# Kernel tuning notes

Hardware: AMD Instinct MI355X
Metric: run time of the kernel (lower is better)

The kernel has to match this reference:

```python
import jax, jax.numpy as jnp
import numpy as np

DIM = 512
HEADS = 8
DIM_HEAD = 64
INNER = HEADS * DIM_HEAD  # 512
B, N = 4, 2048


def setup_inputs() -> dict:
    key = jax.random.key(0)
    k1, k2, k3, k4 = jax.random.split(key, 4)
    x = jax.random.normal(k1, (B, N, DIM), dtype=jnp.float32)
    # nn.Linear(dim, inner*3, bias=False): weight [3*inner, dim]; store transposed [dim, 3*inner]
    w_qkv = jax.random.normal(k2, (DIM, 3 * INNER), dtype=jnp.float32) / np.sqrt(DIM)
    w_out = jax.random.normal(k3, (INNER, DIM), dtype=jnp.float32) / np.sqrt(INNER)
    b_out = jax.random.normal(k4, (DIM,), dtype=jnp.float32) * 0.01
    return {"x": x, "w_qkv": w_qkv, "w_out": w_out, "b_out": b_out}


def reference(x, w_qkv, w_out, b_out):
    b, n, _ = x.shape
    scale = DIM_HEAD ** -0.5
    qkv = x @ w_qkv  # [b, n, 3*inner]
    q, k, v = jnp.split(qkv, 3, axis=-1)
    # [b, n, h, d] -> [b, h, n, d]
    reshape = lambda t: t.reshape(b, n, HEADS, DIM_HEAD).transpose(0, 2, 1, 3)
    q, k, v = reshape(q), reshape(k), reshape(v)
    dots = jnp.einsum('bhid,bhjd->bhij', q, k) * scale  # [b, h, n, n]
    attn = jax.nn.softmax(dots, axis=-1)
    out = jnp.einsum('bhij,bhjd->bhid', attn, v)  # [b, h, n, d]
    out = out.transpose(0, 2, 1, 3).reshape(b, n, INNER)
    return out @ w_out + b_out  # dropout is identity at inference
```

## Files before the change

### kernel.cpp

```cpp
#include <hip/hip_runtime.h>
#include <hip/hip_bf16.h>
#include <cstdint>

#define DEV __device__ __forceinline__

typedef __attribute__((ext_vector_type(8))) __bf16 bf16x8;
typedef __attribute__((ext_vector_type(4))) float floatx4;
typedef __attribute__((ext_vector_type(4))) short shortx4;
typedef __attribute__((ext_vector_type(8))) short shortx8;

constexpr float QSCALE = 0.18033688011112042f;

DEV unsigned short f2b(float f) {
  union { float f; unsigned u; } v; v.f = f;
  return (unsigned short)((v.u + 0x7fffu + ((v.u >> 16) & 1u)) >> 16);
}

#if defined(__has_builtin) && __has_builtin(__builtin_amdgcn_cvt_pk_bf16_f32)
DEV unsigned pk2(float a, float b) {
  typedef __attribute__((ext_vector_type(2))) __bf16 bf2;
  union { bf2 v; unsigned u; } u;
  u.v = __builtin_amdgcn_cvt_pk_bf16_f32(a, b);
  return u.u;
}
#else
DEV unsigned pk2(float a, float b) {
  return (unsigned)f2b(a) | ((unsigned)f2b(b) << 16);
}
#endif

#if defined(__has_builtin) && __has_builtin(__builtin_amdgcn_exp2f)
DEV float fexp2(float x) { return __builtin_amdgcn_exp2f(x); }
#else
DEV float fexp2(float x) { return exp2f(x); }
#endif

DEV floatx4 mfma16(bf16x8 a, bf16x8 b, floatx4 c) {
  return __builtin_amdgcn_mfma_f32_16x16x32_bf16(a, b, c, 0, 0, 0);
}

#define GLD_LDS16(gp, lp)                                                          \
  __builtin_amdgcn_global_load_lds(                                                \
      (const __attribute__((address_space(1))) void*)(gp),                         \
      (__attribute__((address_space(3))) void*)(lp), 16, 0, 0)

__global__ void cvt_f32_bf16(const float* __restrict__ in,
                             unsigned short* __restrict__ out, int n4) {
  int i = blockIdx.x * 256 + threadIdx.x;
  if (i >= n4) return;
  floatx4 f = ((const floatx4*)in)[i];
  shortx4 s;
  s[0] = (short)f2b(f[0]); s[1] = (short)f2b(f[1]);
  s[2] = (short)f2b(f[2]); s[3] = (short)f2b(f[3]);
  ((shortx4*)out)[i] = s;
}

__global__ void tcvt(const float* __restrict__ in, unsigned short* __restrict__ out,
                     int R, int C) {
  __shared__ float tile[32][33];
  int tx = threadIdx.x & 31, ty = threadIdx.x >> 5;
  int r0 = blockIdx.y * 32, c0 = blockIdx.x * 32;
#pragma unroll
  for (int i = 0; i < 4; i++) {
    int rr = ty + i * 8;
    tile[rr][tx] = in[(size_t)(r0 + rr) * C + c0 + tx];
  }
  __syncthreads();
#pragma unroll
  for (int i = 0; i < 4; i++) {
    int rr = ty + i * 8;
    out[(size_t)(c0 + rr) * R + r0 + tx] = f2b(tile[tx][rr]);
  }
}

__global__ void vtrans(const unsigned short* __restrict__ in,
                       unsigned short* __restrict__ out) {
  __shared__ unsigned short Ts[64][68];
  const int t = threadIdx.x;
  const int n0 = blockIdx.x * 64;
  const size_t base = (size_t)blockIdx.y * (2048 * 64);
  const int rr = t >> 4, c4 = (t & 15) * 4;
#pragma unroll
  for (int j = 0; j < 4; j++) {
    int row = j * 16 + rr;
    *(shortx4*)(&Ts[row][c4]) =
        *(const shortx4*)(in + base + (size_t)(n0 + row) * 64 + c4);
  }
  __syncthreads();
#pragma unroll
  for (int j = 0; j < 4; j++) {
    int d = j * 16 + rr;
    shortx4 s;
#pragma unroll
    for (int i = 0; i < 4; i++) s[i] = (short)Ts[c4 + i][d];
    *(shortx4*)(out + base + (size_t)d * 2048 + n0 + c4) = s;
  }
}

template <int MODE>
__global__ __launch_bounds__(256, 2) void gemm_bt(
    const unsigned short* __restrict__ A, const unsigned short* __restrict__ Bt, int K,
    unsigned short* __restrict__ qg, unsigned short* __restrict__ kg,
    unsigned short* __restrict__ vg, float* __restrict__ outF,
    const float* __restrict__ bias) {
  __shared__ __align__(16) unsigned short Xs[128 * 32];
  __shared__ __align__(16) unsigned short Ws[128 * 32];
  const int tid = threadIdx.x;
  const int lane = tid & 63, wid = tid >> 6;
  const int g = lane >> 4, r = lane & 15;
  const int m0 = blockIdx.y * 128, n0 = blockIdx.x * 128;
  const int wm = (wid & 1) * 64, wn = (wid >> 1) * 64;

  floatx4 acc[4][4] = {};

  const int c0i = tid, c1i = 256 + tid;
  const int row0 = c0i >> 2, kb0 = (c0i & 3) ^ ((row0 >> 1) & 3);
  const int row1 = c1i >> 2, kb1 = (c1i & 3) ^ ((row1 >> 1) & 3);
  const unsigned ldsOff0 = (unsigned)(wid * 64) * 16;
  const unsigned ldsOff1 = (unsigned)(256 + wid * 64) * 16;

  for (int kt = 0; kt < K; kt += 32) {
    GLD_LDS16(A + (size_t)(m0 + row0) * K + kt + kb0 * 8, (char*)Xs + ldsOff0);
    GLD_LDS16(A + (size_t)(m0 + row1) * K + kt + kb1 * 8, (char*)Xs + ldsOff1);
    GLD_LDS16(Bt + (size_t)(n0 + row0) * K + kt + kb0 * 8, (char*)Ws + ldsOff0);
    GLD_LDS16(Bt + (size_t)(n0 + row1) * K + kt + kb1 * 8, (char*)Ws + ldsOff1);
    __syncthreads();
    bf16x8 a[4], b[4];
#pragma unroll
    for (int t = 0; t < 4; t++) {
      int rowA = wm + t * 16 + r;
      a[t] = *(const bf16x8*)(Xs + rowA * 32 + (g ^ ((rowA >> 1) & 3)) * 8);
      int rowB = wn + t * 16 + r;
      b[t] = *(const bf16x8*)(Ws + rowB * 32 + (g ^ ((rowB >> 1) & 3)) * 8);
    }
#pragma unroll
    for (int mt = 0; mt < 4; mt++)
#pragma unroll
      for (int nt = 0; nt < 4; nt++)
        acc[mt][nt] = mfma16(a[mt], b[nt], acc[mt][nt]);
    __syncthreads();
  }

#pragma unroll
  for (int mt = 0; mt < 4; mt++)
#pragma unroll
    for (int nt = 0; nt < 4; nt++) {
      int col = n0 + wn + nt * 16 + r;
#pragma unroll
      for (int e = 0; e < 4; e++) {
        int rowm = m0 + wm + mt * 16 + g * 4 + e;
        float v = acc[mt][nt][e];
        if (MODE == 0) {
          int which = col >> 9;
          int h = (col >> 6) & 7, d = col & 63;
          int bb = rowm >> 11, n = rowm & 2047;
          size_t idx = ((size_t)(bb * 8 + h) * 2048 + n) * 64 + d;
          if (which == 0) qg[idx] = f2b(v * QSCALE);
          else if (which == 1) kg[idx] = f2b(v);
          else vg[idx] = f2b(v);
        } else {
          outF[(size_t)rowm * 512 + col] = v + bias[col];
        }
      }
    }
}

__global__ __launch_bounds__(256, 2) void attn(
    const unsigned short* __restrict__ qg, const unsigned short* __restrict__ kg,
    const unsigned short* __restrict__ vtg, unsigned short* __restrict__ ao) {
  __shared__ __align__(16) unsigned short Ks[2 * 64 * 64];
  __shared__ __align__(16) unsigned short Vt[2 * 64 * 64];
  __shared__ __align__(16) unsigned short Pn[4 * 64 * 64];
  const int tid = threadIdx.x, lane = tid & 63, wid = tid >> 6;
  const int g = lane >> 4, r = lane & 15, r7 = r & 7;
  const int wq = wid & 1, wk = wid >> 1;
  const int bh = blockIdx.y, q0 = blockIdx.x * 128;
  const size_t base = (size_t)bh * (2048 * 64);
  const int chunk = (lane & 7) ^ ((lane >> 3) & 7);
  const int srow = lane >> 3;

  bf16x8 bq[4][2];
#pragma unroll
  for (int nt = 0; nt < 4; nt++)
#pragma unroll
    for (int kc = 0; kc < 2; kc++)
      bq[nt][kc] = *(const bf16x8*)(qg + base +
                                    (size_t)(q0 + wq * 64 + nt * 16 + r) * 64 +
                                    kc * 32 + g * 8);

  bf16x8 vones;
#pragma unroll
  for (int i = 0; i < 8; i++) vones[i] = (__bf16)1.0f;

  floatx4 o[4][4] = {};
  floatx4 lacc[4] = {};

  for (int it = 0; it < 16; it++) {
    const int n0 = it * 128 + wk * 64;
    if (it) __syncthreads();
    if (wq == 0) {
#pragma unroll
      for (int j = 0; j < 8; j++) {
        int row = j * 8 + srow;
        GLD_LDS16(kg + base + (size_t)(n0 + row) * 64 + chunk * 8,
                  (char*)Ks + wk * 8192 + j * 1024);
      }
    } else {
#pragma unroll
      for (int j = 0; j < 8; j++) {
        int row = j * 8 + srow;
        GLD_LDS16(vtg + base + (size_t)row * 2048 + n0 + chunk * 8,
                  (char*)Vt + wk * 8192 + j * 1024);
      }
    }
    __syncthreads();

    floatx4 st[4][4] = {};
#pragma unroll
    for (int kc = 0; kc < 2; kc++)
#pragma unroll
      for (int mt = 0; mt < 4; mt++) {
        bf16x8 ak = *(const bf16x8*)(Ks + wk * 4096 + (mt * 16 + r) * 64 +
                                     ((kc * 4 + g) ^ r7) * 8);
#pragma unroll
        for (int nt = 0; nt < 4; nt++)
          st[mt][nt] = mfma16(ak, bq[nt][kc], st[mt][nt]);
      }

#pragma unroll
    for (int mt = 0; mt < 4; mt++)
#pragma unroll
      for (int nt = 0; nt < 4; nt++) {
        unsigned lo = pk2(fexp2(st[mt][nt][0]), fexp2(st[mt][nt][1]));
        unsigned hi = pk2(fexp2(st[mt][nt][2]), fexp2(st[mt][nt][3]));
        unsigned long long w = (unsigned long long)lo |
                               ((unsigned long long)hi << 32);
        int prow = nt * 16 + r;
        int slot = (mt * 2 + (g >> 1)) ^ r7;
        *(unsigned long long*)((char*)Pn + wid * 8192 + prow * 128 + slot * 16 +
                               (g & 1) * 8) = w;
      }

#pragma unroll
    for (int kc = 0; kc < 2; kc++) {
      bf16x8 bv[4];
#pragma unroll
      for (int nt = 0; nt < 4; nt++)
        bv[nt] = *(const bf16x8*)(Vt + wk * 4096 + (nt * 16 + r) * 64 +
                                  ((kc * 4 + g) ^ r7) * 8);
#pragma unroll
      for (int mt = 0; mt < 4; mt++) {
        bf16x8 ap = *(const bf16x8*)(Pn + wid * 4096 + (mt * 16 + r) * 64 +
                                     ((kc * 4 + g) ^ r7) * 8);
        lacc[mt] = mfma16(ap, vones, lacc[mt]);
#pragma unroll
        for (int nt = 0; nt < 4; nt++)
          o[mt][nt] = mfma16(ap, bv[nt], o[mt][nt]);
      }
    }
  }

  __syncthreads();
  float* fP = (float*)Pn;
  float* fL = (float*)Ks;
  if (wk == 1) {
#pragma unroll
    for (int mt = 0; mt < 4; mt++) {
      *(floatx4*)&fL[wq * 1024 + mt * 256 + lane * 4] = lacc[mt];
#pragma unroll
      for (int nt = 0; nt < 4; nt++)
        *(floatx4*)&fP[wq * 4096 + (mt * 4 + nt) * 256 + lane * 4] = o[mt][nt];
    }
  }
  __syncthreads();
  if (wk == 0) {
    const int bb = bh >> 3, h = bh & 7;
#pragma unroll
    for (int mt = 0; mt < 4; mt++) {
      floatx4 lt = lacc[mt] + *(floatx4*)&fL[wq * 1024 + mt * 256 + lane * 4];
      floatx4 il;
#pragma unroll
      for (int e = 0; e < 4; e++) il[e] = 1.f / lt[e];
#pragma unroll
      for (int nt = 0; nt < 4; nt++) {
        floatx4 oo = o[mt][nt] +
                     *(floatx4*)&fP[wq * 4096 + (mt * 4 + nt) * 256 + lane * 4];
        int d = nt * 16 + r;
#pragma unroll
        for (int e = 0; e < 4; e++) {
          int qrow = q0 + wq * 64 + mt * 16 + g * 4 + e;
          ao[((size_t)(bb * 2048 + qrow)) * 512 + h * 64 + d] =
              f2b(oo[e] * il[e]);
        }
      }
    }
  }
}

extern "C" void kernel_launch(void* const* d_in, const int* in_sizes, int n_in,
                              void* d_out, int out_size, void* d_ws, size_t ws_size,
                              hipStream_t stream) {
  const float* x = (const float*)d_in[0];
  const float* w_qkv = (const float*)d_in[1];
  const float* w_out = (const float*)d_in[2];
  const float* b_out = (const float*)d_in[3];
  float* out = (float*)d_out;

  unsigned short* wsp = (unsigned short*)d_ws;
  unsigned short* xb = wsp;
  unsigned short* wqkvt = xb + (size_t)8192 * 512;
  unsigned short* woutt = wqkvt + (size_t)1536 * 512;
  unsigned short* qg = woutt + (size_t)512 * 512;
  unsigned short* kg = qg + (size_t)32 * 2048 * 64;
  unsigned short* vg = kg + (size_t)32 * 2048 * 64;
  unsigned short* vtg = vg + (size_t)32 * 2048 * 64;
  unsigned short* ao = vg;

  cvt_f32_bf16<<<4096, 256, 0, stream>>>(x, xb, 8192 * 512 / 4);
  tcvt<<<dim3(48, 16), 256, 0, stream>>>(w_qkv, wqkvt, 512, 1536);
  tcvt<<<dim3(16, 16), 256, 0, stream>>>(w_out, woutt, 512, 512);
  gemm_bt<0><<<dim3(12, 64), 256, 0, stream>>>(xb, wqkvt, 512, qg, kg, vg,
                                               nullptr, nullptr);
  vtrans<<<dim3(32, 32), 256, 0, stream>>>(vg, vtg);
  attn<<<dim3(16, 32), 256, 0, stream>>>(qg, kg, vtg, ao);
  gemm_bt<1><<<dim3(4, 64), 256, 0, stream>>>(ao, woutt, 512, nullptr, nullptr,
                                              nullptr, out, b_out);
}
```

Baseline: 171.8 us.

## Fuse V transpose into QKV GEMM, register-resident attention, coalesced epilogues

```diff
diff --git a/kernel.cpp b/kernel.cpp
--- a/kernel.cpp
+++ b/kernel.cpp
@@ -73,38 +73,15 @@
   }
 }
 
-__global__ void vtrans(const unsigned short* __restrict__ in,
-                       unsigned short* __restrict__ out) {
-  __shared__ unsigned short Ts[64][68];
-  const int t = threadIdx.x;
-  const int n0 = blockIdx.x * 64;
-  const size_t base = (size_t)blockIdx.y * (2048 * 64);
-  const int rr = t >> 4, c4 = (t & 15) * 4;
-#pragma unroll
-  for (int j = 0; j < 4; j++) {
-    int row = j * 16 + rr;
-    *(shortx4*)(&Ts[row][c4]) =
-        *(const shortx4*)(in + base + (size_t)(n0 + row) * 64 + c4);
-  }
-  __syncthreads();
-#pragma unroll
-  for (int j = 0; j < 4; j++) {
-    int d = j * 16 + rr;
-    shortx4 s;
-#pragma unroll
-    for (int i = 0; i < 4; i++) s[i] = (short)Ts[c4 + i][d];
-    *(shortx4*)(out + base + (size_t)d * 2048 + n0 + c4) = s;
-  }
-}
-
 template <int MODE>
 __global__ __launch_bounds__(256, 2) void gemm_bt(
     const unsigned short* __restrict__ A, const unsigned short* __restrict__ Bt, int K,
     unsigned short* __restrict__ qg, unsigned short* __restrict__ kg,
-    unsigned short* __restrict__ vg, float* __restrict__ outF,
+    unsigned short* __restrict__ vtg, float* __restrict__ outF,
     const float* __restrict__ bias) {
-  __shared__ __align__(16) unsigned short Xs[128 * 32];
-  __shared__ __align__(16) unsigned short Ws[128 * 32];
+  __shared__ __align__(16) unsigned short smem[128 * 136];
+  unsigned short* Xs = smem;
+  unsigned short* Ws = smem + 4096;
   const int tid = threadIdx.x;
   const int lane = tid & 63, wid = tid >> 6;
   const int g = lane >> 4, r = lane & 15;
@@ -141,51 +118,99 @@
     __syncthreads();
   }
 
-#pragma unroll
-  for (int mt = 0; mt < 4; mt++)
-#pragma unroll
-    for (int nt = 0; nt < 4; nt++) {
-      int col = n0 + wn + nt * 16 + r;
-#pragma unroll
-      for (int e = 0; e < 4; e++) {
-        int rowm = m0 + wm + mt * 16 + g * 4 + e;
-        float v = acc[mt][nt][e];
-        if (MODE == 0) {
-          int which = col >> 9;
-          int h = (col >> 6) & 7, d = col & 63;
-          int bb = rowm >> 11, n = rowm & 2047;
-          size_t idx = ((size_t)(bb * 8 + h) * 2048 + n) * 64 + d;
-          if (which == 0) qg[idx] = f2b(v * QSCALE);
-          else if (which == 1) kg[idx] = f2b(v);
-          else vg[idx] = f2b(v);
-        } else {
-          outF[(size_t)rowm * 512 + col] = v + bias[col];
+  if (MODE == 0) {
+    const int which = blockIdx.x >> 2;
+    if (which == 2) {
+      const int tokbase = m0 + wm;
+      const int bb = tokbase >> 11, nb = tokbase & 2047;
+#pragma unroll
+      for (int mt = 0; mt < 4; mt++) {
+        const int s = (mt >> 1) * 32 + g * 8 + (mt & 1) * 4;
+#pragma unroll
+        for (int nt = 0; nt < 4; nt++) {
+          int vcol = n0 + wn + nt * 16 + r - 1024;
+          int h = vcol >> 6, d = vcol & 63;
+          unsigned long long w =
+              (unsigned long long)pk2(acc[mt][nt][0], acc[mt][nt][1]) |
+              ((unsigned long long)pk2(acc[mt][nt][2], acc[mt][nt][3]) << 32);
+          *(unsigned long long*)(vtg + ((size_t)(bb * 8 + h) * 64 + d) * 2048 +
+                                 nb + s) = w;
         }
       }
-    }
-}
-
-__global__ __launch_bounds__(256, 2) void attn(
+    } else {
+      const float sc = (which == 0) ? QSCALE : 1.f;
+      unsigned short* dst = (which == 0) ? qg : kg;
+#pragma unroll
+      for (int mt = 0; mt < 4; mt++)
+#pragma unroll
+        for (int nt = 0; nt < 4; nt++) {
+          int col = wn + nt * 16 + r;
+#pragma unroll
+          for (int e = 0; e < 4; e++) {
+            int row = wm + mt * 16 + g * 4 + e;
+            smem[row * 136 + col] = f2b(acc[mt][nt][e] * sc);
+          }
+        }
+      __syncthreads();
+#pragma unroll
+      for (int it = 0; it < 8; it++) {
+        int c = it * 256 + tid;
+        int row = c >> 4, cc = c & 15;
+        shortx8 v = *(const shortx8*)(smem + row * 136 + cc * 8);
+        int gq = n0 + cc * 8;
+        int h = (gq >> 6) & 7, d0 = gq & 63;
+        int tok = m0 + row, bb = tok >> 11, n = tok & 2047;
+        *(shortx8*)(dst + ((size_t)(bb * 8 + h) * 2048 + n) * 64 + d0) = v;
+      }
+    }
+  } else {
+    float* ftile = (float*)smem;
+#pragma unroll
+    for (int half = 0; half < 2; half++) {
+      if (half) __syncthreads();
+#pragma unroll
+      for (int mi = 0; mi < 2; mi++) {
+        int mt = half * 2 + mi;
+#pragma unroll
+        for (int nt = 0; nt < 4; nt++)
+#pragma unroll
+          for (int e = 0; e < 4; e++) {
+            int lr = (wm >> 1) + mi * 16 + g * 4 + e;
+            ftile[lr * 132 + wn + nt * 16 + r] = acc[mt][nt][e];
+          }
+      }
+      __syncthreads();
+#pragma unroll
+      for (int it = 0; it < 8; it++) {
+        int c = it * 256 + tid;
+        int lr = c >> 5, cc = c & 31;
+        floatx4 v = *(const floatx4*)(ftile + lr * 132 + cc * 4);
+        int col = n0 + cc * 4;
+        v += *(const floatx4*)(bias + col);
+        int rowt = (lr < 32) ? (half * 32 + lr) : (64 + half * 32 + (lr - 32));
+        *(floatx4*)(outF + (size_t)(m0 + rowt) * 512 + col) = v;
+      }
+    }
+  }
+}
+
+__global__ __launch_bounds__(256, 1) void attn(
     const unsigned short* __restrict__ qg, const unsigned short* __restrict__ kg,
     const unsigned short* __restrict__ vtg, unsigned short* __restrict__ ao) {
-  __shared__ __align__(16) unsigned short Ks[2 * 64 * 64];
-  __shared__ __align__(16) unsigned short Vt[2 * 64 * 64];
-  __shared__ __align__(16) unsigned short Pn[4 * 64 * 64];
+  __shared__ __align__(16) unsigned short Os[4][64 * 72];
   const int tid = threadIdx.x, lane = tid & 63, wid = tid >> 6;
-  const int g = lane >> 4, r = lane & 15, r7 = r & 7;
-  const int wq = wid & 1, wk = wid >> 1;
-  const int bh = blockIdx.y, q0 = blockIdx.x * 128;
+  const int g = lane >> 4, r = lane & 15;
+  const int bh = blockIdx.y;
+  const int qw = blockIdx.x * 256 + wid * 64;
   const size_t base = (size_t)bh * (2048 * 64);
-  const int chunk = (lane & 7) ^ ((lane >> 3) & 7);
-  const int srow = lane >> 3;
+  const unsigned short* Vb = vtg + base;
 
   bf16x8 bq[4][2];
 #pragma unroll
   for (int nt = 0; nt < 4; nt++)
 #pragma unroll
     for (int kc = 0; kc < 2; kc++)
-      bq[nt][kc] = *(const bf16x8*)(qg + base +
-                                    (size_t)(q0 + wq * 64 + nt * 16 + r) * 64 +
+      bq[nt][kc] = *(const bf16x8*)(qg + base + (size_t)(qw + nt * 16 + r) * 64 +
                                     kc * 32 + g * 8);
 
   bf16x8 vones;
@@ -195,105 +220,92 @@
   floatx4 o[4][4] = {};
   floatx4 lacc[4] = {};
 
-  for (int it = 0; it < 16; it++) {
-    const int n0 = it * 128 + wk * 64;
-    if (it) __syncthreads();
-    if (wq == 0) {
-#pragma unroll
-      for (int j = 0; j < 8; j++) {
-        int row = j * 8 + srow;
-        GLD_LDS16(kg + base + (size_t)(n0 + row) * 64 + chunk * 8,
-                  (char*)Ks + wk * 8192 + j * 1024);
-      }
-    } else {
-#pragma unroll
-      for (int j = 0; j < 8; j++) {
-        int row = j * 8 + srow;
-        GLD_LDS16(vtg + base + (size_t)row * 2048 + n0 + chunk * 8,
-                  (char*)Vt + wk * 8192 + j * 1024);
-      }
-    }
-    __syncthreads();
+  bf16x8 ak[4][2];
+#pragma unroll
+  for (int mt = 0; mt < 4; mt++)
+#pragma unroll
+    for (int kc = 0; kc < 2; kc++)
+      ak[mt][kc] = *(const bf16x8*)(kg + base + (size_t)(mt * 16 + r) * 64 +
+                                    kc * 32 + g * 8);
+
+  for (int n0 = 0; n0 < 2048; n0 += 64) {
+    bf16x8 bv[4][2];
+#pragma unroll
+    for (int b = 0; b < 4; b++)
+#pragma unroll
+      for (int kc = 0; kc < 2; kc++)
+        bv[b][kc] = *(const bf16x8*)(Vb + (size_t)(b * 16 + r) * 2048 + n0 +
+                                     kc * 32 + g * 8);
 
     floatx4 st[4][4] = {};
 #pragma unroll
     for (int kc = 0; kc < 2; kc++)
 #pragma unroll
-      for (int mt = 0; mt < 4; mt++) {
-        bf16x8 ak = *(const bf16x8*)(Ks + wk * 4096 + (mt * 16 + r) * 64 +
-                                     ((kc * 4 + g) ^ r7) * 8);
+      for (int mt = 0; mt < 4; mt++)
 #pragma unroll
         for (int nt = 0; nt < 4; nt++)
-          st[mt][nt] = mfma16(ak, bq[nt][kc], st[mt][nt]);
-      }
-
-#pragma unroll
-    for (int mt = 0; mt < 4; mt++)
-#pragma unroll
-      for (int nt = 0; nt < 4; nt++) {
-        unsigned lo = pk2(fexp2(st[mt][nt][0]), fexp2(st[mt][nt][1]));
-        unsigned hi = pk2(fexp2(st[mt][nt][2]), fexp2(st[mt][nt][3]));
-        unsigned long long w = (unsigned long long)lo |
-                               ((unsigned long long)hi << 32);
-        int prow = nt * 16 + r;
-        int slot = (mt * 2 + (g >> 1)) ^ r7;
-        *(unsigned long long*)((char*)Pn + wid * 8192 + prow * 128 + slot * 16 +
-                               (g & 1) * 8) = w;
-      }
+          st[mt][nt] = mfma16(ak[mt][kc], bq[nt][kc], st[mt][nt]);
+
+    if (n0 + 64 < 2048) {
+#pragma unroll
+      for (int mt = 0; mt < 4; mt++)
+#pragma unroll
+        for (int kc = 0; kc < 2; kc++)
+          ak[mt][kc] = *(const bf16x8*)(kg + base +
+                                        (size_t)(n0 + 64 + mt * 16 + r) * 64 +
+                                        kc * 32 + g * 8);
+    }
+
+    bf16x8 ap[4][2];
+#pragma unroll
+    for (int a = 0; a < 4; a++) {
+      float p[4][4];
+#pragma unroll
+      for (int mt = 0; mt < 4; mt++)
+#pragma unroll
+        for (int e = 0; e < 4; e++) p[mt][e] = fexp2(st[mt][a][e]);
+#pragma unroll
+      for (int kc = 0; kc < 2; kc++) {
+        union { unsigned u[4]; bf16x8 v; } w;
+        w.u[0] = pk2(p[2 * kc][0], p[2 * kc][1]);
+        w.u[1] = pk2(p[2 * kc][2], p[2 * kc][3]);
+        w.u[2] = pk2(p[2 * kc + 1][0], p[2 * kc + 1][1]);
+        w.u[3] = pk2(p[2 * kc + 1][2], p[2 * kc + 1][3]);
+        ap[a][kc] = w.v;
+      }
+    }
 
 #pragma unroll
     for (int kc = 0; kc < 2; kc++) {
-      bf16x8 bv[4];
-#pragma unroll
-      for (int nt = 0; nt < 4; nt++)
-        bv[nt] = *(const bf16x8*)(Vt + wk * 4096 + (nt * 16 + r) * 64 +
-                                  ((kc * 4 + g) ^ r7) * 8);
-#pragma unroll
-      for (int mt = 0; mt < 4; mt++) {
-        bf16x8 ap = *(const bf16x8*)(Pn + wid * 4096 + (mt * 16 + r) * 64 +
-                                     ((kc * 4 + g) ^ r7) * 8);
-        lacc[mt] = mfma16(ap, vones, lacc[mt]);
-#pragma unroll
-        for (int nt = 0; nt < 4; nt++)
-          o[mt][nt] = mfma16(ap, bv[nt], o[mt][nt]);
-      }
-    }
-  }
-
+#pragma unroll
+      for (int a = 0; a < 4; a++) {
+        lacc[a] = mfma16(ap[a][kc], vones, lacc[a]);
+#pragma unroll
+        for (int b = 0; b < 4; b++)
+          o[a][b] = mfma16(ap[a][kc], bv[b][kc], o[a][b]);
+      }
+    }
+  }
+
+#pragma unroll
+  for (int a = 0; a < 4; a++) {
+    floatx4 il;
+#pragma unroll
+    for (int e = 0; e < 4; e++) il[e] = 1.f / lacc[a][e];
+#pragma unroll
+    for (int b = 0; b < 4; b++)
+#pragma unroll
+      for (int e = 0; e < 4; e++)
+        Os[wid][(a * 16 + g * 4 + e) * 72 + b * 16 + r] = f2b(o[a][b][e] * il[e]);
+  }
   __syncthreads();
-  float* fP = (float*)Pn;
-  float* fL = (float*)Ks;
-  if (wk == 1) {
-#pragma unroll
-    for (int mt = 0; mt < 4; mt++) {
-      *(floatx4*)&fL[wq * 1024 + mt * 256 + lane * 4] = lacc[mt];
-#pragma unroll
-      for (int nt = 0; nt < 4; nt++)
-        *(floatx4*)&fP[wq * 4096 + (mt * 4 + nt) * 256 + lane * 4] = o[mt][nt];
-    }
-  }
-  __syncthreads();
-  if (wk == 0) {
-    const int bb = bh >> 3, h = bh & 7;
-#pragma unroll
-    for (int mt = 0; mt < 4; mt++) {
-      floatx4 lt = lacc[mt] + *(floatx4*)&fL[wq * 1024 + mt * 256 + lane * 4];
-      floatx4 il;
-#pragma unroll
-      for (int e = 0; e < 4; e++) il[e] = 1.f / lt[e];
-#pragma unroll
-      for (int nt = 0; nt < 4; nt++) {
-        floatx4 oo = o[mt][nt] +
-                     *(floatx4*)&fP[wq * 4096 + (mt * 4 + nt) * 256 + lane * 4];
-        int d = nt * 16 + r;
-#pragma unroll
-        for (int e = 0; e < 4; e++) {
-          int qrow = q0 + wq * 64 + mt * 16 + g * 4 + e;
-          ao[((size_t)(bb * 2048 + qrow)) * 512 + h * 64 + d] =
-              f2b(oo[e] * il[e]);
-        }
-      }
-    }
+  const int bb = bh >> 3, h = bh & 7;
+#pragma unroll
+  for (int it = 0; it < 8; it++) {
+    int c = it * 64 + lane;
+    int row = c >> 3, cc = c & 7;
+    shortx8 v = *(const shortx8*)(&Os[wid][row * 72 + cc * 8]);
+    *(shortx8*)(ao + ((size_t)(bb * 2048 + qw + row)) * 512 + h * 64 + cc * 8) = v;
   }
 }
 
@@ -312,17 +324,15 @@
   unsigned short* woutt = wqkvt + (size_t)1536 * 512;
   unsigned short* qg = woutt + (size_t)512 * 512;
   unsigned short* kg = qg + (size_t)32 * 2048 * 64;
-  unsigned short* vg = kg + (size_t)32 * 2048 * 64;
-  unsigned short* vtg = vg + (size_t)32 * 2048 * 64;
-  unsigned short* ao = vg;
+  unsigned short* vtg = kg + (size_t)32 * 2048 * 64;
+  unsigned short* ao = vtg + (size_t)32 * 2048 * 64;
 
   cvt_f32_bf16<<<4096, 256, 0, stream>>>(x, xb, 8192 * 512 / 4);
   tcvt<<<dim3(48, 16), 256, 0, stream>>>(w_qkv, wqkvt, 512, 1536);
   tcvt<<<dim3(16, 16), 256, 0, stream>>>(w_out, woutt, 512, 512);
-  gemm_bt<0><<<dim3(12, 64), 256, 0, stream>>>(xb, wqkvt, 512, qg, kg, vg,
+  gemm_bt<0><<<dim3(12, 64), 256, 0, stream>>>(xb, wqkvt, 512, qg, kg, vtg,
                                                nullptr, nullptr);
-  vtrans<<<dim3(32, 32), 256, 0, stream>>>(vg, vtg);
-  attn<<<dim3(16, 32), 256, 0, stream>>>(qg, kg, vtg, ao);
+  attn<<<dim3(8, 32), 256, 0, stream>>>(qg, kg, vtg, ao);
   gemm_bt<1><<<dim3(4, 64), 256, 0, stream>>>(ao, woutt, 512, nullptr, nullptr,
                                               nullptr, out, b_out);
 }
```

Measured after the change: 180.6 us. +5.1%, slower.
